# Kernel tuning notes

Measured on AMD Instinct MI355X. Metric: run time of the kernel, lower is better.

## Reference

```python
import jax, jax.numpy as jnp
import numpy as np

N_NODES = 10000
N_PAIRS = 1200000
DIM = 128


def setup_inputs() -> dict:
    key = jax.random.key(0)
    k1, k2, k3, k4, k5, k6, k7 = jax.random.split(key, 7)
    features = jax.random.normal(k1, (N_NODES, DIM), dtype=jnp.float32)
    dist = jax.random.uniform(k2, (N_NODES, N_NODES), dtype=jnp.float32)
    pair_node = jnp.sort(jax.random.randint(k3, (N_PAIRS,), 0, N_NODES, dtype=jnp.int32))
    pair_i = jax.random.randint(k4, (N_PAIRS,), 0, N_NODES, dtype=jnp.int32)
    pair_j = jax.random.randint(k5, (N_PAIRS,), 0, N_NODES, dtype=jnp.int32)
    # cosine-like values in [-1, 1]
    pair_cos = jax.random.uniform(k6, (N_PAIRS,), dtype=jnp.float32, minval=-1.0, maxval=1.0)
    # xavier_uniform for (input_dim, output_dim)
    limit = float(np.sqrt(6.0 / (DIM + DIM)))
    W = jax.random.uniform(k7, (DIM, DIM), dtype=jnp.float32, minval=-limit, maxval=limit)
    b = jnp.zeros((DIM,), dtype=jnp.float32)
    return {"features": features, "dist": dist, "pair_node": pair_node,
            "pair_i": pair_i, "pair_j": pair_j, "pair_cos": pair_cos,
            "W": W, "b": b}


def reference(features, dist, pair_node, pair_i, pair_j, pair_cos, W, b):
    # scalar weight per pair: cos(i,j around node) * dist[node,i] * dist[node,j]
    w = pair_cos * dist[pair_node, pair_i] * dist[pair_node, pair_j]  # [P]
    # per-pair contribution: (f_i + f_j) * w
    contrib = (features[pair_i] + features[pair_j]) * w[:, None]  # [P, D]
    agg = jax.ops.segment_sum(contrib, pair_node, num_segments=N_NODES)  # [N, D]
    return agg @ W + b
```

## Files before the change

kernel.cpp:

```cpp
#include <hip/hip_runtime.h>

#define N_NODES 10000
#define N_PAIRS 1200000
#define DIM 128

__device__ inline float bf2f(unsigned short u) {
    return __uint_as_float(((unsigned int)u) << 16);
}
__device__ inline unsigned short f2bf(float f) {
    unsigned int i = __float_as_uint(f);
    unsigned int r = i + 0x7FFFu + ((i >> 16) & 1u);
    return (unsigned short)(r >> 16);
}
__device__ inline float rl_f(float v, int q) {
    return __uint_as_float(__builtin_amdgcn_readlane(__float_as_uint(v), q));
}

__global__ __launch_bounds__(256)
void seg_start_kernel(const int* __restrict__ pair_node, int* __restrict__ seg) {
    const int p = blockIdx.x * 256 + threadIdx.x;
    if (p >= N_PAIRS) return;
    const int cur  = pair_node[p];
    const int prev = (p == 0) ? -1 : pair_node[p - 1];
    for (int n = prev + 1; n <= cur; ++n) seg[n] = p;
    if (p == N_PAIRS - 1)
        for (int n = cur + 1; n <= N_NODES; ++n) seg[n] = N_PAIRS;
}

__global__ __launch_bounds__(256, 4)
void fw_gemm_kernel(const float* __restrict__ F, const float* __restrict__ W,
                    ushort2* __restrict__ FWb2)
{
    const int wid  = threadIdx.x >> 6;
    const int lane = threadIdx.x & 63;
    const int m0   = (blockIdx.x * 4 + wid) * 4;
    if (m0 >= N_NODES) return;

    const float2* F2 = (const float2*)F;
    const float2* W2 = (const float2*)W;

    const float2 f0 = F2[(size_t)(m0 + 0) * 64 + lane];
    const float2 f1 = F2[(size_t)(m0 + 1) * 64 + lane];
    const float2 f2 = F2[(size_t)(m0 + 2) * 64 + lane];
    const float2 f3 = F2[(size_t)(m0 + 3) * 64 + lane];

    float2 a0 = {0.f, 0.f}, a1 = {0.f, 0.f}, a2 = {0.f, 0.f}, a3 = {0.f, 0.f};

    #pragma unroll 4
    for (int kk = 0; kk < 64; ++kk) {
        const float2 wa = W2[(size_t)(2 * kk + 0) * 64 + lane];
        const float2 wb = W2[(size_t)(2 * kk + 1) * 64 + lane];
        const float s0x = rl_f(f0.x, kk), s0y = rl_f(f0.y, kk);
        const float s1x = rl_f(f1.x, kk), s1y = rl_f(f1.y, kk);
        const float s2x = rl_f(f2.x, kk), s2y = rl_f(f2.y, kk);
        const float s3x = rl_f(f3.x, kk), s3y = rl_f(f3.y, kk);
        a0.x += s0x * wa.x + s0y * wb.x;  a0.y += s0x * wa.y + s0y * wb.y;
        a1.x += s1x * wa.x + s1y * wb.x;  a1.y += s1x * wa.y + s1y * wb.y;
        a2.x += s2x * wa.x + s2y * wb.x;  a2.y += s2x * wa.y + s2y * wb.y;
        a3.x += s3x * wa.x + s3y * wb.x;  a3.y += s3x * wa.y + s3y * wb.y;
    }

    ushort2 o;
    o.x = f2bf(a0.x); o.y = f2bf(a0.y); FWb2[(size_t)(m0 + 0) * 64 + lane] = o;
    o.x = f2bf(a1.x); o.y = f2bf(a1.y); FWb2[(size_t)(m0 + 1) * 64 + lane] = o;
    o.x = f2bf(a2.x); o.y = f2bf(a2.y); FWb2[(size_t)(m0 + 2) * 64 + lane] = o;
    o.x = f2bf(a3.x); o.y = f2bf(a3.y); FWb2[(size_t)(m0 + 3) * 64 + lane] = o;
}

__global__ __launch_bounds__(256, 8)
void fused_seg_kernel(const float* __restrict__ dist,
                      const ushort2* __restrict__ FW2,
                      const int* __restrict__ seg,
                      const int* __restrict__ pair_i,
                      const int* __restrict__ pair_j,
                      const float* __restrict__ pair_cos,
                      const float* __restrict__ b,
                      float* __restrict__ out)
{
    const int wid  = threadIdx.x >> 6;
    const int lane = threadIdx.x & 63;
    const int n    = blockIdx.x * 4 + wid;
    const int lo = seg[n];
    const int hi = seg[n + 1];
    const size_t drow = (size_t)n * N_NODES;

    float a0 = 0.f, a1 = 0.f;

    for (int base = lo; base < hi; base += 64) {
        const int p = base + lane;
        int il = 0, jl = 0; float wl = 0.f;
        if (p < hi) {
            il = pair_i[p];
            jl = pair_j[p];
            wl = pair_cos[p] * dist[drow + il] * dist[drow + jl];
        }

        const int qmax = min(64, hi - base);
        if (qmax == 64) {
            #pragma unroll 8
            for (int q = 0; q < 64; ++q) {
                const int   iq = __builtin_amdgcn_readlane(il, q);
                const int   jq = __builtin_amdgcn_readlane(jl, q);
                const float wq = rl_f(wl, q);
                const ushort2 fi = FW2[(size_t)iq * 64 + lane];
                const ushort2 fj = FW2[(size_t)jq * 64 + lane];
                a0 += wq * (bf2f(fi.x) + bf2f(fj.x));
                a1 += wq * (bf2f(fi.y) + bf2f(fj.y));
            }
        } else {
            #pragma unroll 4
            for (int q = 0; q < qmax; ++q) {
                const int   iq = __builtin_amdgcn_readlane(il, q);
                const int   jq = __builtin_amdgcn_readlane(jl, q);
                const float wq = rl_f(wl, q);
                const ushort2 fi = FW2[(size_t)iq * 64 + lane];
                const ushort2 fj = FW2[(size_t)jq * 64 + lane];
                a0 += wq * (bf2f(fi.x) + bf2f(fj.x));
                a1 += wq * (bf2f(fi.y) + bf2f(fj.y));
            }
        }
    }

    const float2 bb = ((const float2*)b)[lane];
    float2 o; o.x = a0 + bb.x; o.y = a1 + bb.y;
    ((float2*)out)[(size_t)n * 64 + lane] = o;
}

extern "C" void kernel_launch(void* const* d_in, const int* in_sizes, int n_in,
                              void* d_out, int out_size, void* d_ws, size_t ws_size,
                              hipStream_t stream) {
    const float* features  = (const float*)d_in[0];
    const float* dist      = (const float*)d_in[1];
    const int*   pair_node = (const int*)  d_in[2];
    const int*   pair_i    = (const int*)  d_in[3];
    const int*   pair_j    = (const int*)  d_in[4];
    const float* pair_cos  = (const float*)d_in[5];
    const float* W         = (const float*)d_in[6];
    const float* b         = (const float*)d_in[7];
    float* out = (float*)d_out;

    int* seg = (int*)d_ws;
    ushort2* FWb2 = (ushort2*)((char*)d_ws + 10240 * sizeof(int));

    seg_start_kernel<<<(N_PAIRS + 255) / 256, 256, 0, stream>>>(pair_node, seg);
    fw_gemm_kernel<<<(N_NODES / 16 + 0), 256, 0, stream>>>(features, W, FWb2);
    fused_seg_kernel<<<N_NODES / 4, 256, 0, stream>>>(
        dist, FWb2, seg, pair_i, pair_j, pair_cos, b, out);
}
```

Before: 103.7 us.

## Stage dist rows in LDS, split each node across eight waves, merge prep kernels

The segment-start and feature-times-W prep kernels become one launch that branches on block index. The aggregation kernel now gives each node a 512-thread block. The block copies the node's full dist row into shared memory with coalesced float4 loads, so the per-pair dist lookups no longer go out to global memory as random gathers. The node's pairs are split across eight waves and their partial sums are reduced through shared memory. This adds parallelism per node and cuts gather latency, but it reads the entire dense dist matrix instead of only the entries touched. The 40KB of shared memory per block also limits occupancy.

After: 163.1 us. 1.57x slower.

```diff
diff --git a/kernel.cpp b/kernel.cpp
--- a/kernel.cpp
+++ b/kernel.cpp
@@ -3,37 +3,42 @@
 #define N_NODES 10000
 #define N_PAIRS 1200000
 #define DIM 128
+#define ROW4 2500
+#define SEG_BLOCKS 4688
+#define FW_BLOCKS 625
 
 __device__ inline float bf2f(unsigned short u) {
     return __uint_as_float(((unsigned int)u) << 16);
 }
 __device__ inline unsigned short f2bf(float f) {
     unsigned int i = __float_as_uint(f);
-    unsigned int r = i + 0x7FFFu + ((i >> 16) & 1u);
-    return (unsigned short)(r >> 16);
+    return (unsigned short)((i + 0x7FFFu + ((i >> 16) & 1u)) >> 16);
 }
 __device__ inline float rl_f(float v, int q) {
     return __uint_as_float(__builtin_amdgcn_readlane(__float_as_uint(v), q));
 }
 
-__global__ __launch_bounds__(256)
-void seg_start_kernel(const int* __restrict__ pair_node, int* __restrict__ seg) {
-    const int p = blockIdx.x * 256 + threadIdx.x;
-    if (p >= N_PAIRS) return;
-    const int cur  = pair_node[p];
-    const int prev = (p == 0) ? -1 : pair_node[p - 1];
-    for (int n = prev + 1; n <= cur; ++n) seg[n] = p;
-    if (p == N_PAIRS - 1)
-        for (int n = cur + 1; n <= N_NODES; ++n) seg[n] = N_PAIRS;
-}
+__global__ __launch_bounds__(256, 4)
+void prep_kernel(const int* __restrict__ pair_node, int* __restrict__ seg,
+                 const float* __restrict__ F, const float* __restrict__ W,
+                 ushort2* __restrict__ FWb2)
+{
+    const int bid = blockIdx.x;
+    if (bid < SEG_BLOCKS) {
+        const int p = bid * 256 + threadIdx.x;
+        if (p >= N_PAIRS) return;
+        const int cur  = pair_node[p];
+        const int prev = (p == 0) ? -1 : pair_node[p - 1];
+        for (int n = prev + 1; n <= cur; ++n) seg[n] = p;
+        if (p == N_PAIRS - 1)
+            for (int n = cur + 1; n <= N_NODES; ++n) seg[n] = N_PAIRS;
+        return;
+    }
 
-__global__ __launch_bounds__(256, 4)
-void fw_gemm_kernel(const float* __restrict__ F, const float* __restrict__ W,
-                    ushort2* __restrict__ FWb2)
-{
+    const int fb   = bid - SEG_BLOCKS;
     const int wid  = threadIdx.x >> 6;
     const int lane = threadIdx.x & 63;
-    const int m0   = (blockIdx.x * 4 + wid) * 4;
+    const int m0   = (fb * 4 + wid) * 4;
     if (m0 >= N_NODES) return;
 
     const float2* F2 = (const float2*)F;
@@ -67,63 +72,76 @@
     o.x = f2bf(a3.x); o.y = f2bf(a3.y); FWb2[(size_t)(m0 + 3) * 64 + lane] = o;
 }
 
-__global__ __launch_bounds__(256, 8)
-void fused_seg_kernel(const float* __restrict__ dist,
-                      const ushort2* __restrict__ FW2,
-                      const int* __restrict__ seg,
-                      const int* __restrict__ pair_i,
-                      const int* __restrict__ pair_j,
-                      const float* __restrict__ pair_cos,
-                      const float* __restrict__ b,
-                      float* __restrict__ out)
+__global__ __launch_bounds__(512, 4)
+void fused_kernel(const float* __restrict__ dist,
+                  const ushort2* __restrict__ FW2,
+                  const int* __restrict__ seg,
+                  const int* __restrict__ pair_i,
+                  const int* __restrict__ pair_j,
+                  const float* __restrict__ pair_cos,
+                  const float* __restrict__ b,
+                  float* __restrict__ out)
 {
-    const int wid  = threadIdx.x >> 6;
-    const int lane = threadIdx.x & 63;
-    const int n    = blockIdx.x * 4 + wid;
-    const int lo = seg[n];
-    const int hi = seg[n + 1];
-    const size_t drow = (size_t)n * N_NODES;
+    __shared__ float sRow[N_NODES];
+
+    const int n    = blockIdx.x;
+    const int tid  = threadIdx.x;
+    const int wid  = tid >> 6;
+    const int lane = tid & 63;
+
+    const float4* dist4 = (const float4*)dist + (size_t)n * ROW4;
+    float4* sRow4 = (float4*)sRow;
+    for (int t = tid; t < ROW4; t += 512)
+        sRow4[t] = dist4[t];
+
+    const int lo  = seg[n];
+    const int hi  = seg[n + 1];
+
+    __syncthreads();
 
     float a0 = 0.f, a1 = 0.f;
 
-    for (int base = lo; base < hi; base += 64) {
-        const int p = base + lane;
+    for (int base = lo; base < hi; base += 512) {
+        const int m   = min(512, hi - base);
+        const int per = (m + 7) >> 3;
+        const int s   = base + wid * per;
+        const int myc = max(0, min(s + per, base + m) - s);
+
         int il = 0, jl = 0; float wl = 0.f;
-        if (p < hi) {
+        if (lane < myc) {
+            const int p = s + lane;
             il = pair_i[p];
             jl = pair_j[p];
-            wl = pair_cos[p] * dist[drow + il] * dist[drow + jl];
+            wl = pair_cos[p] * sRow[il] * sRow[jl];
         }
 
-        const int qmax = min(64, hi - base);
-        if (qmax == 64) {
-            #pragma unroll 8
-            for (int q = 0; q < 64; ++q) {
-                const int   iq = __builtin_amdgcn_readlane(il, q);
-                const int   jq = __builtin_amdgcn_readlane(jl, q);
-                const float wq = rl_f(wl, q);
-                const ushort2 fi = FW2[(size_t)iq * 64 + lane];
-                const ushort2 fj = FW2[(size_t)jq * 64 + lane];
-                a0 += wq * (bf2f(fi.x) + bf2f(fj.x));
-                a1 += wq * (bf2f(fi.y) + bf2f(fj.y));
-            }
-        } else {
-            #pragma unroll 4
-            for (int q = 0; q < qmax; ++q) {
-                const int   iq = __builtin_amdgcn_readlane(il, q);
-                const int   jq = __builtin_amdgcn_readlane(jl, q);
-                const float wq = rl_f(wl, q);
-                const ushort2 fi = FW2[(size_t)iq * 64 + lane];
-                const ushort2 fj = FW2[(size_t)jq * 64 + lane];
-                a0 += wq * (bf2f(fi.x) + bf2f(fj.x));
-                a1 += wq * (bf2f(fi.y) + bf2f(fj.y));
-            }
+        #pragma unroll 4
+        for (int q = 0; q < myc; ++q) {
+            const int   iq = __builtin_amdgcn_readlane(il, q);
+            const int   jq = __builtin_amdgcn_readlane(jl, q);
+            const float wq = rl_f(wl, q);
+            const ushort2 fi = FW2[(size_t)iq * 64 + lane];
+            const ushort2 fj = FW2[(size_t)jq * 64 + lane];
+            a0 += wq * (bf2f(fi.x) + bf2f(fj.x));
+            a1 += wq * (bf2f(fi.y) + bf2f(fj.y));
         }
     }
 
-    const float2 bb = ((const float2*)b)[lane];
-    float2 o; o.x = a0 + bb.x; o.y = a1 + bb.y;
-    ((float2*)out)[(size_t)n * 64 + lane] = o;
+    __syncthreads();
+    float2* sAcc2 = (float2*)sRow;
+    sAcc2[wid * 64 + lane] = make_float2(a0, a1);
+    __syncthreads();
+
+    if (tid < 64) {
+        float2 t = sAcc2[tid];
+        #pragma unroll
+        for (int w2 = 1; w2 < 8; ++w2) {
+            const float2 v = sAcc2[w2 * 64 + tid];
+            t.x += v.x; t.y += v.y;
+        }
+        const float2 bb = ((const float2*)b)[tid];
+        ((float2*)out)[(size_t)n * 64 + tid] = make_float2(t.x + bb.x, t.y + bb.y);
+    }
 }
 
 extern "C" void kernel_launch(void* const* d_in, const int* in_sizes, int n_in,
@@ -142,8 +160,7 @@
     int* seg = (int*)d_ws;
     ushort2* FWb2 = (ushort2*)((char*)d_ws + 10240 * sizeof(int));
 
-    seg_start_kernel<<<(N_PAIRS + 255) / 256, 256, 0, stream>>>(pair_node, seg);
-    fw_gemm_kernel<<<(N_NODES / 16 + 0), 256, 0, stream>>>(features, W, FWb2);
-    fused_seg_kernel<<<N_NODES / 4, 256, 0, stream>>>(
+    prep_kernel<<<SEG_BLOCKS + FW_BLOCKS, 256, 0, stream>>>(pair_node, seg, features, W, FWb2);
+    fused_kernel<<<N_NODES, 512, 0, stream>>>(
         dist, FWb2, seg, pair_i, pair_j, pair_cos, b, out);
 }
```
